# Kernel optimization log

Measured on AMD Instinct MI355X. Metric: run time of the kernel, lower is better.

The kernel has to match this reference:

```python
import jax, jax.numpy as jnp
import numpy as np

N = 50000        # vertices
E = 1_600_000    # edges (avg degree 32)
CIN = 8          # in_channels (scalar input features)
COUT = 32        # out_channels (tangent vector channels, complex -> trailing dim 2)
R = 2            # n_corr_rings (radial profile rings)
EPS = 1e-6


def setup_inputs() -> dict:
    key = jax.random.key(0)
    ks = jax.random.split(key, 12)
    x = jax.random.normal(ks[0], (N, CIN), jnp.float32)
    edge_index = jax.random.randint(ks[1], (2, E), 0, N, dtype=jnp.int32)
    # precomputed per-edge transport * radial interpolation coefficients (re, im) per ring
    pcmp_gather = jax.random.normal(ks[2], (E, R, 2), jnp.float32)
    # TransField learned radial profile and phase offset (offset=True)
    W_rad = jax.random.normal(ks[3], (R, CIN, COUT), jnp.float32) / np.float32(np.sqrt(R * CIN))
    phase = jax.random.normal(ks[4], (COUT,), jnp.float32)
    # TangentNonLin bias after the field conv
    b_nl = jax.random.normal(ks[5], (COUT,), jnp.float32) * 0.1
    # three TangentPerceptrons: complex-linear (real weight shared over re/im) + TangentNonLin
    sc = np.float32(1.0 / np.sqrt(COUT))
    W1 = jax.random.normal(ks[6], (COUT, COUT), jnp.float32) * sc
    b1 = jax.random.normal(ks[7], (COUT,), jnp.float32) * 0.1
    W2 = jax.random.normal(ks[8], (COUT, COUT), jnp.float32) * sc
    b2 = jax.random.normal(ks[9], (COUT,), jnp.float32) * 0.1
    W3 = jax.random.normal(ks[10], (COUT, COUT), jnp.float32) * sc
    b3 = jax.random.normal(ks[11], (COUT,), jnp.float32) * 0.1
    return dict(x=x, edge_index=edge_index, pcmp_gather=pcmp_gather, W_rad=W_rad,
                phase=phase, b_nl=b_nl, W1=W1, b1=b1, W2=W2, b2=b2, W3=W3, b3=b3)


def tangent_nonlin(z, b):
    # ReLU on magnitude with learned per-channel bias, phase preserved
    mag = jnp.sqrt(jnp.sum(z * z, axis=-1) + EPS)           # [N, C]
    scale = jax.nn.relu(mag + b) / mag                      # [N, C]
    return z * scale[..., None]


def trans_field(x, src, dst, pcmp_gather, W_rad, phase, n_nodes):
    xs = x[src]                                             # gather: [E, CIN]
    t = jnp.einsum('ei,rio->ero', xs, W_rad)                # [E, R, COUT]
    # modulate by complex transport coeffs per ring, sum rings -> [E, COUT, 2]
    msg = jnp.sum(t[..., None] * pcmp_gather[:, :, None, :], axis=1)
    agg = jax.ops.segment_sum(msg, dst, num_segments=n_nodes)  # scatter: [N, COUT, 2]
    # learned phase offset: rotate each output channel by e^{i*phase}
    c, s = jnp.cos(phase), jnp.sin(phase)
    re = agg[..., 0] * c - agg[..., 1] * s
    im = agg[..., 0] * s + agg[..., 1] * c
    return jnp.stack([re, im], axis=-1)                     # [N, COUT, 2]


def reference(x, edge_index, pcmp_gather, W_rad, phase, b_nl, W1, b1, W2, b2, W3, b3):
    src, dst = edge_index[0], edge_index[1]
    y = trans_field(x, src, dst, pcmp_gather, W_rad, phase, x.shape[0])
    y = tangent_nonlin(y, b_nl)
    for W, b in ((W1, b1), (W2, b2), (W3, b3)):
        y = jnp.einsum('nik,io->nok', y, W)                 # complex-linear (shared real weight)
        y = tangent_nonlin(y, b)
    return y
```

## Files before the change

kernel.cpp:

```cpp
#include <hip/hip_runtime.h>

#define CIN 8
#define COUT 32
#define NR 2
#define EPSF 1e-6f

#define BSH 5
#define BNODES 32
#define NBMAX 2048
#define CHUNK 8192
#define IDBITS 21
#define IDMASK ((1u << IDBITS) - 1u)
#define SRCMASK 0x03FFFFFFu
#define PSTAGE 2560
#define AREG (PSTAGE / 256)

__global__ __launch_bounds__(256) void bucket_hist(
    const int* __restrict__ eidx, int* __restrict__ bucketCnt, int E, int nb)
{
    __shared__ int cnt[NBMAX];
    for (int i = threadIdx.x; i < nb; i += 256) cnt[i] = 0;
    __syncthreads();
    for (int e = blockIdx.x * 256 + threadIdx.x; e < E; e += gridDim.x * 256)
        atomicAdd(&cnt[eidx[E + e] >> BSH], 1);
    __syncthreads();
    for (int i = threadIdx.x; i < nb; i += 256)
        if (cnt[i]) atomicAdd(&bucketCnt[i], cnt[i]);
}

__global__ __launch_bounds__(1024) void scan_init(
    const int* __restrict__ bucketCnt, int* __restrict__ bucketBase,
    int* __restrict__ gCursor, int nb)
{
    __shared__ int sA[NBMAX], sB[NBMAX];
    for (int i = threadIdx.x; i < NBMAX; i += 1024)
        sA[i] = (i < nb) ? bucketCnt[i] : 0;
    __syncthreads();
    int* src = sA; int* dst = sB;
    for (int off = 1; off < NBMAX; off <<= 1) {
        for (int i = threadIdx.x; i < NBMAX; i += 1024)
            dst[i] = src[i] + (i >= off ? src[i - off] : 0);
        __syncthreads();
        int* tmp = src; src = dst; dst = tmp;
    }
    for (int i = threadIdx.x; i < nb; i += 1024) {
        int incl = src[i];
        int base = incl - bucketCnt[i];
        bucketBase[i] = base;
        gCursor[i] = base;
        if (i == nb - 1) bucketBase[nb] = incl;
    }
}

template<bool PACKED>
__global__ __launch_bounds__(256) void binify(
    const int* __restrict__ eidx, int* __restrict__ gCursor,
    unsigned* __restrict__ outMeta,
    float4*   __restrict__ pcmpS,
    const float* __restrict__ pcmp, int E, int nb)
{
    __shared__ int cnt[NBMAX];
    __shared__ int sA[NBMAX], sB[NBMAX];
    __shared__ int gbase[NBMAX];
    __shared__ unsigned sid[CHUNK];

    const int e0 = blockIdx.x * CHUNK;
    const int num = min(CHUNK, E - e0);

    for (int i = threadIdx.x; i < nb; i += 256) cnt[i] = 0;
    __syncthreads();
    for (int k = threadIdx.x; k < num; k += 256)
        atomicAdd(&cnt[eidx[E + e0 + k] >> BSH], 1);
    __syncthreads();

    for (int j = threadIdx.x; j < NBMAX; j += 256) sA[j] = (j < nb) ? cnt[j] : 0;
    __syncthreads();
    int* src = sA; int* dstp = sB;
    for (int off = 1; off < NBMAX; off <<= 1) {
        for (int j = threadIdx.x; j < NBMAX; j += 256)
            dstp[j] = src[j] + (j >= off ? src[j - off] : 0);
        __syncthreads();
        int* tmp = src; src = dstp; dstp = tmp;
    }

    for (int b = threadIdx.x; b < nb; b += 256)
        gbase[b] = atomicAdd(&gCursor[b], cnt[b]);
    __syncthreads();
    for (int i = threadIdx.x; i < nb; i += 256) cnt[i] = 0;
    __syncthreads();

    for (int k = threadIdx.x; k < num; k += 256) {
        int e = e0 + k;
        int d = eidx[E + e];
        int b = d >> BSH;
        int slot = (b ? src[b - 1] : 0) + atomicAdd(&cnt[b], 1);
        sid[slot] = ((unsigned)(d & (BNODES - 1)) << IDBITS) | (unsigned)e;
    }
    __syncthreads();

    for (int s = threadIdx.x; s < num; s += 256) {
        int lo = 0, hi = nb;
        while (lo < hi) { int mid = (lo + hi) >> 1; if (src[mid] > s) hi = mid; else lo = mid + 1; }
        int b = lo;
        int intra = s - (b ? src[b - 1] : 0);
        unsigned v = sid[s];
        int pos = gbase[b] + intra;
        if (PACKED) {
            int id = v & IDMASK;
            unsigned dl = v >> IDBITS;
            unsigned sv = (unsigned)eidx[id];
            outMeta[pos] = (dl << 26) | sv;
            pcmpS[pos] = *reinterpret_cast<const float4*>(pcmp + (size_t)id * 4);
        } else {
            outMeta[pos] = v;
        }
    }
}

template<bool SRC16>
__global__ __launch_bounds__(256) void fused_staged_kernel(
    const float* __restrict__ x,
    const float4* __restrict__ pcmpS,
    const unsigned* __restrict__ meta,
    const int* __restrict__ bucketBase,
    const float* __restrict__ W_rad, const float* __restrict__ phase,
    const float* __restrict__ b_nl,
    const float* __restrict__ W1, const float* __restrict__ b1,
    const float* __restrict__ W2, const float* __restrict__ b2,
    const float* __restrict__ W3, const float* __restrict__ b3,
    float* __restrict__ out, int N)
{
    __shared__ float sWrad[NR * CIN][COUT];
    __shared__ float sW[3][COUT][COUT];
    __shared__ float sPh[COUT][2];
    __shared__ float sBias[4][COUT];
    __shared__ float pcfL[4][PSTAGE + 8];
    __shared__ unsigned short srcL16[SRC16 ? PSTAGE : 2];
    __shared__ unsigned srcL32[SRC16 ? 2 : PSTAGE];
    __shared__ int cnt[BNODES], segS[BNODES], cur[BNODES], padL[BNODES];
    __shared__ int totPad;

    for (int i = threadIdx.x; i < NR * CIN * COUT; i += 256) ((float*)sWrad)[i] = W_rad[i];
    for (int i = threadIdx.x; i < COUT * COUT; i += 256) {
        ((float*)sW[0])[i] = W1[i];
        ((float*)sW[1])[i] = W2[i];
        ((float*)sW[2])[i] = W3[i];
    }
    if (threadIdx.x < COUT) {
        float sn, cs; __sincosf(phase[threadIdx.x], &sn, &cs);
        sPh[threadIdx.x][0] = cs; sPh[threadIdx.x][1] = sn;
        sBias[0][threadIdx.x] = b_nl[threadIdx.x];
        sBias[1][threadIdx.x] = b1[threadIdx.x];
        sBias[2][threadIdx.x] = b2[threadIdx.x];
        sBias[3][threadIdx.x] = b3[threadIdx.x];
    }
    if (threadIdx.x < BNODES) cnt[threadIdx.x] = 0;

    const int start = bucketBase[blockIdx.x];
    const int total = bucketBase[blockIdx.x + 1] - start;
    const bool ovf0 = (total > PSTAGE);
    if (threadIdx.x == 0) totPad = ovf0 ? 0x7FFFFFFF : 0;
    __syncthreads();

    unsigned mreg[AREG];
    float4   preg[AREG];
    const int staged = ovf0 ? 0 : total;
#pragma unroll
    for (int kk = 0; kk < AREG; ++kk) {
        int k = threadIdx.x + (kk << 8);
        if (k < staged) {
            mreg[kk] = meta[start + k];
            preg[kk] = pcmpS[start + k];
            atomicAdd(&cnt[mreg[kk] >> 26], 1);
        }
    }
    __syncthreads();

    if (threadIdx.x < BNODES) {
        int v = cnt[threadIdx.x];
        int m = v;
        m = max(m, __shfl_xor(m, 1, 32));
        m = max(m, __shfl_xor(m, 2, 32));
        int pl = (m + 3) & ~3;
        int incl = pl;
#pragma unroll
        for (int off = 1; off < BNODES; off <<= 1) {
            int u = __shfl_up(incl, off, 32);
            if ((int)threadIdx.x >= off) incl += u;
        }
        segS[threadIdx.x] = incl - pl;
        cur[threadIdx.x]  = incl - pl;
        padL[threadIdx.x] = pl;
        if (threadIdx.x == BNODES - 1 && !ovf0) totPad = incl;
    }
    __syncthreads();

    const bool fb = (totPad > PSTAGE);

    if (!fb) {
#pragma unroll
        for (int kk = 0; kk < AREG; ++kk) {
            int k = threadIdx.x + (kk << 8);
            if (k < staged) {
                unsigned m = mreg[kk];
                int pos = atomicAdd(&cur[m >> 26], 1);
                if (SRC16) srcL16[pos] = (unsigned short)(m & 0xFFFFu);
                else       srcL32[pos] = m & SRCMASK;
                pcfL[0][pos] = preg[kk].x;
                pcfL[1][pos] = preg[kk].y;
                pcfL[2][pos] = preg[kk].z;
                pcfL[3][pos] = preg[kk].w;
            }
        }
        if (threadIdx.x < BNODES) {
            int p0 = segS[threadIdx.x] + cnt[threadIdx.x];
            int p1 = segS[threadIdx.x] + padL[threadIdx.x];
            for (int p = p0; p < p1; ++p) {
                if (SRC16) srcL16[p] = 0; else srcL32[p] = 0;
                pcfL[0][p] = 0.f; pcfL[1][p] = 0.f;
                pcfL[2][p] = 0.f; pcfL[3][p] = 0.f;
            }
        }
    }
    __syncthreads();

    const int c   = threadIdx.x & 31;
    const int sub = threadIdx.x >> 5;
    const int i_idx  = (c >> 1) & 7;
    const int pc_off = ((c >> 4) << 1) | (c & 1);
    const int node0 = blockIdx.x << BSH;
    const int gl0 = sub * 4;

    float qs[4];
    if (!fb) {
        const float* pcrow = &pcfL[pc_off][0];
        const int T  = padL[gl0];
        const int b0 = segS[gl0 + 0];
        const int b1 = segS[gl0 + 1];
        const int b2 = segS[gl0 + 2];
        const int b3 = segS[gl0 + 3];
        float q0 = 0.f, q1 = 0.f, q2 = 0.f, q3 = 0.f;
#pragma unroll 2
        for (int t = 0; t < T; ++t) {
            int s0, s1, s2, s3;
            if (SRC16) {
                s0 = srcL16[b0 + t]; s1 = srcL16[b1 + t];
                s2 = srcL16[b2 + t]; s3 = srcL16[b3 + t];
            } else {
                s0 = (int)srcL32[b0 + t]; s1 = (int)srcL32[b1 + t];
                s2 = (int)srcL32[b2 + t]; s3 = (int)srcL32[b3 + t];
            }
            float c0 = pcrow[b0 + t], c1 = pcrow[b1 + t];
            float c2 = pcrow[b2 + t], c3 = pcrow[b3 + t];
            q0 += x[(s0 << 3) + i_idx] * c0;
            q1 += x[(s1 << 3) + i_idx] * c1;
            q2 += x[(s2 << 3) + i_idx] * c2;
            q3 += x[(s3 << 3) + i_idx] * c3;
        }
        qs[0] = q0; qs[1] = q1; qs[2] = q2; qs[3] = q3;
    } else {
        const float* pcfG = (const float*)(pcmpS + start);
#pragma unroll
        for (int r = 0; r < 4; ++r) {
            const int gl = gl0 + r;
            float q = 0.f;
            for (int t = 0; t < total; ++t) {
                unsigned m = meta[start + t];
                if ((int)(m >> 26) == gl)
                    q += x[(size_t)(m & SRCMASK) * CIN + i_idx] * pcfG[(t << 2) | pc_off];
            }
            qs[r] = q;
        }
    }

#pragma unroll
    for (int r = 0; r < 4; ++r) {
        const int n = node0 + gl0 + r;
        float a0 = 0.f, a1 = 0.f;
#pragma unroll
        for (int ri = 0; ri < NR * CIN; ++ri) {
            float w = sWrad[ri][c];
            a0 += w * __shfl(qs[r], 2 * ri,     32);
            a1 += w * __shfl(qs[r], 2 * ri + 1, 32);
        }
        float cs = sPh[c][0], sn = sPh[c][1];
        float re = a0 * cs - a1 * sn;
        float im = a0 * sn + a1 * cs;
        float mag = sqrtf(re * re + im * im + EPSF);
        float sc  = fmaxf(mag + sBias[0][c], 0.f) / mag;
        re *= sc; im *= sc;
#pragma unroll
        for (int L = 0; L < 3; ++L) {
            float bb0 = 0.f, bb1 = 0.f;
#pragma unroll
            for (int i = 0; i < COUT; ++i) {
                float w = sW[L][i][c];
                bb0 += w * __shfl(re, i, 32);
                bb1 += w * __shfl(im, i, 32);
            }
            float m2 = sqrtf(bb0 * bb0 + bb1 * bb1 + EPSF);
            float s2 = fmaxf(m2 + sBias[L + 1][c], 0.f) / m2;
            re = bb0 * s2; im = bb1 * s2;
        }
        if (n < N) {
            float2 v; v.x = re; v.y = im;
            *reinterpret_cast<float2*>(out + ((n << 6) + (c << 1))) = v;
        }
    }
}

__global__ __launch_bounds__(256) void fused_bucket_fallback(
    const float* __restrict__ x, const int* __restrict__ eidx,
    const float* __restrict__ pcmp, const int* __restrict__ bucketBase,
    const unsigned* __restrict__ sorted,
    const float* __restrict__ W_rad, const float* __restrict__ phase,
    const float* __restrict__ b_nl,
    const float* __restrict__ W1, const float* __restrict__ b1,
    const float* __restrict__ W2, const float* __restrict__ b2,
    const float* __restrict__ W3, const float* __restrict__ b3,
    float* __restrict__ out, int N)
{
    __shared__ float Q[BNODES][COUT];
    __shared__ float sWrad[NR * CIN][COUT];
    __shared__ float sW[3][COUT][COUT];
    __shared__ float sPh[COUT][2];
    __shared__ float sBias[4][COUT];

    for (int i = threadIdx.x; i < BNODES * COUT; i += 256) ((float*)Q)[i] = 0.f;
    for (int i = threadIdx.x; i < NR * CIN * COUT; i += 256) ((float*)sWrad)[i] = W_rad[i];
    for (int i = threadIdx.x; i < COUT * COUT; i += 256) {
        ((float*)sW[0])[i] = W1[i];
        ((float*)sW[1])[i] = W2[i];
        ((float*)sW[2])[i] = W3[i];
    }
    if (threadIdx.x < COUT) {
        float sn, cs; __sincosf(phase[threadIdx.x], &sn, &cs);
        sPh[threadIdx.x][0] = cs; sPh[threadIdx.x][1] = sn;
        sBias[0][threadIdx.x] = b_nl[threadIdx.x];
        sBias[1][threadIdx.x] = b1[threadIdx.x];
        sBias[2][threadIdx.x] = b2[threadIdx.x];
        sBias[3][threadIdx.x] = b3[threadIdx.x];
    }
    __syncthreads();

    const int c   = threadIdx.x & 31;
    const int sub = threadIdx.x >> 5;
    const int i_idx  = (c >> 1) & 7;
    const int pc_off = ((c >> 4) << 1) | (c & 1);
    const int start = bucketBase[blockIdx.x];
    const int end   = bucketBase[blockIdx.x + 1];

    for (int p = start + sub; p < end; p += 8) {
        unsigned v0 = sorted[p];
        int id0 = v0 & IDMASK;
        int s0 = eidx[id0];
        atomicAdd(&Q[v0 >> IDBITS][c],
                  x[(size_t)s0 * CIN + i_idx] * pcmp[(size_t)id0 * 4 + pc_off]);
    }
    __syncthreads();

    const int node0 = blockIdx.x << BSH;
#pragma unroll
    for (int r = 0; r < 4; ++r) {
        const int gl = r * 8 + sub;
        const int n  = node0 + gl;
        float a0 = 0.f, a1 = 0.f;
#pragma unroll
        for (int ri = 0; ri < NR * CIN; ++ri) {
            float w = sWrad[ri][c];
            a0 += w * Q[gl][2 * ri];
            a1 += w * Q[gl][2 * ri + 1];
        }
        float cs = sPh[c][0], sn = sPh[c][1];
        float re = a0 * cs - a1 * sn;
        float im = a0 * sn + a1 * cs;
        float mag = sqrtf(re * re + im * im + EPSF);
        float sc  = fmaxf(mag + sBias[0][c], 0.f) / mag;
        re *= sc; im *= sc;
#pragma unroll
        for (int L = 0; L < 3; ++L) {
            float b0 = 0.f, b1v = 0.f;
#pragma unroll
            for (int i = 0; i < COUT; ++i) {
                float w = sW[L][i][c];
                b0  += w * __shfl(re, i, 32);
                b1v += w * __shfl(im, i, 32);
            }
            float m2 = sqrtf(b0 * b0 + b1v * b1v + EPSF);
            float s2 = fmaxf(m2 + sBias[L + 1][c], 0.f) / m2;
            re = b0 * s2; im = b1v * s2;
        }
        if (n < N) {
            float2 v; v.x = re; v.y = im;
            *reinterpret_cast<float2*>(out + ((size_t)n * COUT + c) * 2) = v;
        }
    }
}

extern "C" void kernel_launch(void* const* d_in, const int* in_sizes, int n_in,
                              void* d_out, int out_size, void* d_ws, size_t ws_size,
                              hipStream_t stream)
{
    const float* x     = (const float*)d_in[0];
    const int*   eidx  = (const int*)  d_in[1];
    const float* pcmp  = (const float*)d_in[2];
    const float* W_rad = (const float*)d_in[3];
    const float* phase = (const float*)d_in[4];
    const float* b_nl  = (const float*)d_in[5];
    const float* W1    = (const float*)d_in[6];
    const float* b1    = (const float*)d_in[7];
    const float* W2    = (const float*)d_in[8];
    const float* b2    = (const float*)d_in[9];
    const float* W3    = (const float*)d_in[10];
    const float* b3    = (const float*)d_in[11];
    float* out = (float*)d_out;

    const int N = in_sizes[0] / CIN;
    const int E = in_sizes[1] / 2;
    const int nb = (N + BNODES - 1) >> BSH;
    const int nchunk = (E + CHUNK - 1) / CHUNK;

    float4*   pcmpS      = (float4*)d_ws;
    unsigned* meta       = (unsigned*)(pcmpS + E);
    int*      bucketCnt  = (int*)(meta + E);
    int*      bucketBase = bucketCnt + NBMAX;
    int*      gCursor    = bucketBase + NBMAX + 1;
    size_t needed = (size_t)((char*)(gCursor + NBMAX) - (char*)d_ws);

    if (ws_size >= needed) {
        hipMemsetAsync(bucketCnt, 0, (size_t)nb * sizeof(int), stream);
        bucket_hist<<<256, 256, 0, stream>>>(eidx, bucketCnt, E, nb);
        scan_init<<<1, 1024, 0, stream>>>(bucketCnt, bucketBase, gCursor, nb);
        binify<true><<<nchunk, 256, 0, stream>>>(eidx, gCursor, meta, pcmpS, pcmp, E, nb);
        if (N <= 65536) {
            fused_staged_kernel<true><<<nb, 256, 0, stream>>>(
                x, pcmpS, meta, bucketBase,
                W_rad, phase, b_nl, W1, b1, W2, b2, W3, b3, out, N);
        } else {
            fused_staged_kernel<false><<<nb, 256, 0, stream>>>(
                x, pcmpS, meta, bucketBase,
                W_rad, phase, b_nl, W1, b1, W2, b2, W3, b3, out, N);
        }
    } else {
        int*      bc = (int*)d_ws;
        int*      bb = bc + NBMAX;
        int*      gc = bb + NBMAX + 1;
        unsigned* so = (unsigned*)(gc + NBMAX);
        hipMemsetAsync(bc, 0, (size_t)nb * sizeof(int), stream);
        bucket_hist<<<256, 256, 0, stream>>>(eidx, bc, E, nb);
        scan_init<<<1, 1024, 0, stream>>>(bc, bb, gc, nb);
        binify<false><<<nchunk, 256, 0, stream>>>(eidx, gc, so, nullptr, pcmp, E, nb);
        fused_bucket_fallback<<<nb, 256, 0, stream>>>(
            x, eidx, pcmp, bb, so,
            W_rad, phase, b_nl, W1, b1, W2, b2, W3, b3, out, N);
    }
}
```

Baseline: 203.9 us.

## Assign one 8-lane team per node with float4 coefficient staging

The edge-gather loop is reorganised so each 8-lane team owns one destination node. Each lane loads one x feature per edge and applies all four ring/complex coefficients from a single float4 LDS read, instead of four separate gathers with one FMA each. Partial sums go through a shared Qbuf instead of lane shuffles, padding is aligned to the max over 8-node groups, and the LDS staging size is reduced. The smaller staging buffer and wider padding group raise the chance of hitting the slow global fallback path on heavy buckets.

```diff
diff --git a/kernel.cpp b/kernel.cpp
--- a/kernel.cpp
+++ b/kernel.cpp
@@ -12,7 +12,7 @@
 #define IDBITS 21
 #define IDMASK ((1u << IDBITS) - 1u)
 #define SRCMASK 0x03FFFFFFu
-#define PSTAGE 2560
+#define PSTAGE 1792
 #define AREG (PSTAGE / 256)
 
 __global__ __launch_bounds__(256) void bucket_hist(
@@ -118,7 +118,7 @@
 }
 
 template<bool SRC16>
-__global__ __launch_bounds__(256) void fused_staged_kernel(
+__global__ __launch_bounds__(256) void fused_team_kernel(
     const float* __restrict__ x,
     const float4* __restrict__ pcmpS,
     const unsigned* __restrict__ meta,
@@ -134,10 +134,11 @@
     __shared__ float sW[3][COUT][COUT];
     __shared__ float sPh[COUT][2];
     __shared__ float sBias[4][COUT];
-    __shared__ float pcfL[4][PSTAGE + 8];
+    __shared__ float4 pcL[PSTAGE];
     __shared__ unsigned short srcL16[SRC16 ? PSTAGE : 2];
     __shared__ unsigned srcL32[SRC16 ? 2 : PSTAGE];
-    __shared__ int cnt[BNODES], segS[BNODES], cur[BNODES], padL[BNODES];
+    __shared__ float Qbuf[BNODES][33];
+    __shared__ int cnt[BNODES], segS[BNODES], padL[BNODES], cur[BNODES];
     __shared__ int totPad;
 
     for (int i = threadIdx.x; i < NR * CIN * COUT; i += 256) ((float*)sWrad)[i] = W_rad[i];
@@ -181,7 +182,8 @@
         int m = v;
         m = max(m, __shfl_xor(m, 1, 32));
         m = max(m, __shfl_xor(m, 2, 32));
-        int pl = (m + 3) & ~3;
+        m = max(m, __shfl_xor(m, 4, 32));
+        int pl = m;
         int incl = pl;
 #pragma unroll
         for (int off = 1; off < BNODES; off <<= 1) {
@@ -206,82 +208,72 @@
                 int pos = atomicAdd(&cur[m >> 26], 1);
                 if (SRC16) srcL16[pos] = (unsigned short)(m & 0xFFFFu);
                 else       srcL32[pos] = m & SRCMASK;
-                pcfL[0][pos] = preg[kk].x;
-                pcfL[1][pos] = preg[kk].y;
-                pcfL[2][pos] = preg[kk].z;
-                pcfL[3][pos] = preg[kk].w;
+                pcL[pos] = preg[kk];
             }
         }
         if (threadIdx.x < BNODES) {
             int p0 = segS[threadIdx.x] + cnt[threadIdx.x];
             int p1 = segS[threadIdx.x] + padL[threadIdx.x];
+            float4 z = {0.f, 0.f, 0.f, 0.f};
             for (int p = p0; p < p1; ++p) {
                 if (SRC16) srcL16[p] = 0; else srcL32[p] = 0;
-                pcfL[0][p] = 0.f; pcfL[1][p] = 0.f;
-                pcfL[2][p] = 0.f; pcfL[3][p] = 0.f;
+                pcL[p] = z;
             }
         }
     }
     __syncthreads();
 
-    const int c   = threadIdx.x & 31;
-    const int sub = threadIdx.x >> 5;
-    const int i_idx  = (c >> 1) & 7;
-    const int pc_off = ((c >> 4) << 1) | (c & 1);
+    const int c    = threadIdx.x & 31;
+    const int sub  = threadIdx.x >> 5;
+    const int team = c >> 3;
+    const int il   = c & 7;
+    const int gl   = sub * 4 + team;
     const int node0 = blockIdx.x << BSH;
-    const int gl0 = sub * 4;
-
-    float qs[4];
+
+    float4 qa = {0.f, 0.f, 0.f, 0.f};
     if (!fb) {
-        const float* pcrow = &pcfL[pc_off][0];
-        const int T  = padL[gl0];
-        const int b0 = segS[gl0 + 0];
-        const int b1 = segS[gl0 + 1];
-        const int b2 = segS[gl0 + 2];
-        const int b3 = segS[gl0 + 3];
-        float q0 = 0.f, q1 = 0.f, q2 = 0.f, q3 = 0.f;
-#pragma unroll 2
+        const int base = segS[gl];
+        const int T = padL[gl];
+#pragma unroll 4
         for (int t = 0; t < T; ++t) {
-            int s0, s1, s2, s3;
-            if (SRC16) {
-                s0 = srcL16[b0 + t]; s1 = srcL16[b1 + t];
-                s2 = srcL16[b2 + t]; s3 = srcL16[b3 + t];
-            } else {
-                s0 = (int)srcL32[b0 + t]; s1 = (int)srcL32[b1 + t];
-                s2 = (int)srcL32[b2 + t]; s3 = (int)srcL32[b3 + t];
+            int sv = SRC16 ? (int)srcL16[base + t] : (int)srcL32[base + t];
+            float4 pc4 = pcL[base + t];
+            float xf = x[(sv << 3) + il];
+            qa.x += xf * pc4.x;
+            qa.y += xf * pc4.y;
+            qa.z += xf * pc4.z;
+            qa.w += xf * pc4.w;
+        }
+    } else {
+        const float4* pcG = pcmpS + start;
+        for (int t = 0; t < total; ++t) {
+            unsigned m = meta[start + t];
+            if ((int)(m >> 26) == gl) {
+                float4 pc4 = pcG[t];
+                float xf = x[(size_t)(m & SRCMASK) * CIN + il];
+                qa.x += xf * pc4.x;
+                qa.y += xf * pc4.y;
+                qa.z += xf * pc4.z;
+                qa.w += xf * pc4.w;
             }
-            float c0 = pcrow[b0 + t], c1 = pcrow[b1 + t];
-            float c2 = pcrow[b2 + t], c3 = pcrow[b3 + t];
-            q0 += x[(s0 << 3) + i_idx] * c0;
-            q1 += x[(s1 << 3) + i_idx] * c1;
-            q2 += x[(s2 << 3) + i_idx] * c2;
-            q3 += x[(s3 << 3) + i_idx] * c3;
-        }
-        qs[0] = q0; qs[1] = q1; qs[2] = q2; qs[3] = q3;
-    } else {
-        const float* pcfG = (const float*)(pcmpS + start);
-#pragma unroll
-        for (int r = 0; r < 4; ++r) {
-            const int gl = gl0 + r;
-            float q = 0.f;
-            for (int t = 0; t < total; ++t) {
-                unsigned m = meta[start + t];
-                if ((int)(m >> 26) == gl)
-                    q += x[(size_t)(m & SRCMASK) * CIN + i_idx] * pcfG[(t << 2) | pc_off];
-            }
-            qs[r] = q;
-        }
-    }
+        }
+    }
+
+    Qbuf[gl][2 * il]      = qa.x;
+    Qbuf[gl][2 * il + 1]  = qa.y;
+    Qbuf[gl][16 + 2 * il] = qa.z;
+    Qbuf[gl][17 + 2 * il] = qa.w;
 
 #pragma unroll
     for (int r = 0; r < 4; ++r) {
-        const int n = node0 + gl0 + r;
+        const int gln = sub * 4 + r;
+        const int n   = node0 + gln;
         float a0 = 0.f, a1 = 0.f;
 #pragma unroll
         for (int ri = 0; ri < NR * CIN; ++ri) {
             float w = sWrad[ri][c];
-            a0 += w * __shfl(qs[r], 2 * ri,     32);
-            a1 += w * __shfl(qs[r], 2 * ri + 1, 32);
+            a0 += w * Qbuf[gln][2 * ri];
+            a1 += w * Qbuf[gln][2 * ri + 1];
         }
         float cs = sPh[c][0], sn = sPh[c][1];
         float re = a0 * cs - a1 * sn;
@@ -433,11 +425,11 @@
         scan_init<<<1, 1024, 0, stream>>>(bucketCnt, bucketBase, gCursor, nb);
         binify<true><<<nchunk, 256, 0, stream>>>(eidx, gCursor, meta, pcmpS, pcmp, E, nb);
         if (N <= 65536) {
-            fused_staged_kernel<true><<<nb, 256, 0, stream>>>(
+            fused_team_kernel<true><<<nb, 256, 0, stream>>>(
                 x, pcmpS, meta, bucketBase,
                 W_rad, phase, b_nl, W1, b1, W2, b2, W3, b3, out, N);
         } else {
-            fused_staged_kernel<false><<<nb, 256, 0, stream>>>(
+            fused_team_kernel<false><<<nb, 256, 0, stream>>>(
                 x, pcmpS, meta, bucketBase,
                 W_rad, phase, b_nl, W1, b1, W2, b2, W3, b3, out, N);
         }
```

New measurement: 189.4 us. 7.1% less time.
